# Performance work log

Measured on AMD Instinct MI355X. Metric: run time of the kernel, lower is better.

The kernel has to match this reference:

```python
import jax, jax.numpy as jnp
import numpy as np

N = 50000
E = 800000
DIM = 256
H = 8
D = DIM // H


def setup_inputs() -> dict:
    key = jax.random.key(0)
    ks = jax.random.split(key, 12)
    s = 1.0 / np.sqrt(DIM)
    return {
        "x": jax.random.normal(ks[0], (N, DIM), dtype=jnp.float32),
        "Wq": jax.random.normal(ks[1], (DIM, DIM), dtype=jnp.float32) * s,
        "bq": jax.random.normal(ks[2], (DIM,), dtype=jnp.float32) * 0.01,
        "Wk": jax.random.normal(ks[3], (DIM, DIM), dtype=jnp.float32) * s,
        "bk": jax.random.normal(ks[4], (DIM,), dtype=jnp.float32) * 0.01,
        "Wv": jax.random.normal(ks[5], (DIM, DIM), dtype=jnp.float32) * s,
        "bv": jax.random.normal(ks[6], (DIM,), dtype=jnp.float32) * 0.01,
        "Wo": jax.random.normal(ks[7], (DIM, DIM), dtype=jnp.float32) * s,
        "bo": jax.random.normal(ks[8], (DIM,), dtype=jnp.float32) * 0.01,
        "src": jax.random.randint(ks[9], (E,), 0, N, dtype=jnp.int32),
        "dst": jax.random.randint(ks[10], (E,), 0, N, dtype=jnp.int32),
    }


def reference(x, Wq, bq, Wk, bk, Wv, bv, Wo, bo, src, dst):
    # Linear projections (torch Linear: x @ W.T + b), then [N, H, D]
    q = (x @ Wq.T + bq).reshape(N, H, D)
    k = (x @ Wk.T + bk).reshape(N, H, D)
    v = (x @ Wv.T + bv).reshape(N, H, D)

    # u_dot_v: per-edge dot(queries[src], keys[dst]) -> [E, H]
    scores = jnp.einsum('ehd,ehd->eh', q[src], k[dst]) / jnp.sqrt(jnp.float32(D))

    # edge_softmax over incoming edges of each destination node
    smax = jax.ops.segment_max(scores, dst, num_segments=N)  # [N, H]
    e = jnp.exp(scores - smax[dst])                          # [E, H]
    ssum = jax.ops.segment_sum(e, dst, num_segments=N)       # [N, H]
    probs = e / ssum[dst]                                    # [E, H]

    # u_mul_e_sum: sum over incoming edges of values[src] * probs -> [N, H, D]
    out = jax.ops.segment_sum(v[src] * probs[:, :, None], dst, num_segments=N)

    out = out.reshape(N, DIM)
    return out @ Wo.T + bo  # dropout is identity at p=0 / eval
```

## Files before the change

### kernel.cpp

```cpp
#include <hip/hip_runtime.h>
#include <hip/hip_bf16.h>
#include <math.h>

#define DIMV 256
#define DV 32

typedef __attribute__((ext_vector_type(8))) short bf16x8;
typedef __attribute__((ext_vector_type(4))) float f32x4;

static __device__ __forceinline__ unsigned short f2bf(float f) {
    unsigned x = __float_as_uint(f);
    x += 0x7FFF + ((x >> 16) & 1);
    return (unsigned short)(x >> 16);
}
static __device__ __forceinline__ float bf2f(unsigned short u) {
    return __uint_as_float(((unsigned)u) << 16);
}

static __device__ __forceinline__ void async16(const void* g, void* lds) {
    __builtin_amdgcn_global_load_lds(
        (const __attribute__((address_space(1))) void*)g,
        (__attribute__((address_space(3))) void*)lds, 16, 0, 0);
}


__global__ void cvt_w(const float* __restrict__ Wq, const float* __restrict__ Wk,
                      const float* __restrict__ Wv, const float* __restrict__ Wo,
                      unsigned short* __restrict__ Wcat) {
    const float* W = blockIdx.y == 0 ? Wq : blockIdx.y == 1 ? Wk : blockIdx.y == 2 ? Wv : Wo;
    int i = blockIdx.x * 256 + threadIdx.x;
    float4 v = ((const float4*)W)[i];
    ushort4 o;
    o.x = f2bf(v.x); o.y = f2bf(v.y); o.z = f2bf(v.z); o.w = f2bf(v.w);
    ((ushort4*)(Wcat + (size_t)blockIdx.y * 65536))[i] = o;
}


__global__ void zero_i32(int* __restrict__ p, int n) {
    int i = blockIdx.x * blockDim.x + threadIdx.x;
    if (i < n) p[i] = 0;
}

__global__ void count_deg(const int* __restrict__ dst, int* __restrict__ deg, int E) {
    int i = blockIdx.x * blockDim.x + threadIdx.x;
    if (i < E) atomicAdd(&deg[dst[i]], 1);
}

__global__ void block_sum(const int* __restrict__ deg, int* __restrict__ bsum, int n) {
    __shared__ int sm[256];
    int i = blockIdx.x * 256 + threadIdx.x;
    sm[threadIdx.x] = (i < n) ? deg[i] : 0;
    __syncthreads();
    for (int s = 128; s > 0; s >>= 1) {
        if (threadIdx.x < s) sm[threadIdx.x] += sm[threadIdx.x + s];
        __syncthreads();
    }
    if (threadIdx.x == 0) bsum[blockIdx.x] = sm[0];
}

__global__ void scan_bsum(int* __restrict__ bsum, int nb) {
    if (threadIdx.x == 0) {
        int r = 0;
        for (int i = 0; i < nb; ++i) { int v = bsum[i]; bsum[i] = r; r += v; }
    }
}

__global__ void scan_final(const int* __restrict__ deg, const int* __restrict__ bsum,
                           int* __restrict__ offsets, int* __restrict__ cursor, int n) {
    __shared__ int sm[256];
    int i = blockIdx.x * 256 + threadIdx.x;
    int v = (i < n) ? deg[i] : 0;
    sm[threadIdx.x] = v;
    __syncthreads();
    for (int s = 1; s < 256; s <<= 1) {
        int t = (threadIdx.x >= s) ? sm[threadIdx.x - s] : 0;
        __syncthreads();
        sm[threadIdx.x] += t;
        __syncthreads();
    }
    int excl = sm[threadIdx.x] - v + bsum[blockIdx.x];
    if (i < n) { offsets[i] = excl; cursor[i] = excl; }
    if (i == n - 1) offsets[n] = excl + v;
}

__global__ void scatter_edges(const int* __restrict__ src, const int* __restrict__ dst,
                              int* __restrict__ cursor, int* __restrict__ perm_src, int E) {
    int i = blockIdx.x * blockDim.x + threadIdx.x;
    if (i < E) {
        int pos = atomicAdd(&cursor[dst[i]], 1);
        perm_src[pos] = src[i];
    }
}


template<bool AF32, bool OF32>
__global__ __launch_bounds__(256, 4)
void gemm_fused(const void* __restrict__ Ain,
                const unsigned short* __restrict__ Wcat,
                const float* __restrict__ b0, const float* __restrict__ b1,
                const float* __restrict__ b2,
                void* __restrict__ Cout, int M, int ntiles) {
    __shared__ unsigned short Bls[2][32 * 256];
    const int tid = threadIdx.x;
    const int w = tid >> 6, lane = tid & 63;
    const int rg = w >> 1, cg = w & 1;
    const int lrow = lane & 15, lkg = lane >> 4;
    const int row0 = blockIdx.x * 64;

    {
        const char* gb = (const char*)Wcat;
        #pragma unroll
        for (int i = 0; i < 4; ++i) {
            unsigned o = (unsigned)(i * 4096 + w * 1024 + lane * 16);
            unsigned srcoff = o ^ (((o >> 9) & 7u) << 4);
            async16(gb + srcoff, (char*)&Bls[0][0] + (i * 4096 + w * 1024));
        }
    }

    bf16x8 a[2][8];
    #pragma unroll
    for (int m = 0; m < 2; ++m) {
        int row = row0 + rg * 32 + m * 16 + lrow;
        row = min(row, M - 1);
        if (AF32) {
            const float* ap = (const float*)Ain + (size_t)row * DIMV + lkg * 8;
            #pragma unroll
            for (int k0 = 0; k0 < 8; ++k0) {
                float4 f0 = *(const float4*)(ap + k0 * 32);
                float4 f1 = *(const float4*)(ap + k0 * 32 + 4);
                bf16x8 r;
                r[0] = (short)f2bf(f0.x); r[1] = (short)f2bf(f0.y);
                r[2] = (short)f2bf(f0.z); r[3] = (short)f2bf(f0.w);
                r[4] = (short)f2bf(f1.x); r[5] = (short)f2bf(f1.y);
                r[6] = (short)f2bf(f1.z); r[7] = (short)f2bf(f1.w);
                a[m][k0] = r;
            }
        } else {
            const unsigned short* ap = (const unsigned short*)Ain + (size_t)row * DIMV + lkg * 8;
            #pragma unroll
            for (int k0 = 0; k0 < 8; ++k0)
                a[m][k0] = *(const bf16x8*)(ap + k0 * 32);
        }
    }
    __syncthreads();

    const int c = cg * 16 + lrow;
    for (int t = 0; t < ntiles; ++t) {
        if (t + 1 < ntiles) {
            const char* gb = (const char*)Wcat + (size_t)(t + 1) * 16384;
            #pragma unroll
            for (int i = 0; i < 4; ++i) {
                unsigned o = (unsigned)(i * 4096 + w * 1024 + lane * 16);
                unsigned srcoff = o ^ (((o >> 9) & 7u) << 4);
                async16(gb + srcoff, (char*)&Bls[(t + 1) & 1][0] + (i * 4096 + w * 1024));
            }
        }

        const char* bls = (const char*)&Bls[t & 1][0];
        f32x4 acc0 = {0.f, 0.f, 0.f, 0.f};
        f32x4 acc1 = {0.f, 0.f, 0.f, 0.f};
        #pragma unroll
        for (int k0 = 0; k0 < 8; ++k0) {
            unsigned lin = (unsigned)c * 512 + (unsigned)k0 * 64 + (unsigned)lkg * 16;
            unsigned addr = lin ^ (((unsigned)c & 7u) << 4);
            bf16x8 bf = *(const bf16x8*)(bls + addr);
            acc0 = __builtin_amdgcn_mfma_f32_16x16x32_bf16(a[0][k0], bf, acc0, 0, 0, 0);
            acc1 = __builtin_amdgcn_mfma_f32_16x16x32_bf16(a[1][k0], bf, acc1, 0, 0, 0);
        }

        int mat = t >> 3;
        const float* bp = (mat == 0) ? b0 : (mat == 1 ? b1 : b2);
        int gcol = ((t & 7) << 5) + c;
        float bias = bp[gcol];
        size_t obase = (size_t)mat * M * DIMV;
        #pragma unroll
        for (int m = 0; m < 2; ++m) {
            f32x4 av = m ? acc1 : acc0;
            #pragma unroll
            for (int r = 0; r < 4; ++r) {
                int row = row0 + rg * 32 + m * 16 + lkg * 4 + r;
                if (row < M) {
                    float val = av[r] + bias;
                    if (OF32)
                        ((float*)Cout)[obase + (size_t)row * DIMV + gcol] = val;
                    else
                        ((unsigned short*)Cout)[obase + (size_t)row * DIMV + gcol] = f2bf(val);
                }
            }
        }
        __syncthreads();
    }
}


__global__ __launch_bounds__(256)
void node_attn(const unsigned short* __restrict__ Q, const unsigned short* __restrict__ K,
               const unsigned short* __restrict__ V,
               const int* __restrict__ offsets, const int* __restrict__ perm_src,
               unsigned short* __restrict__ attn, int N) {
    int wid = blockIdx.x * (blockDim.x >> 6) + (threadIdx.x >> 6);
    if (wid >= N) return;
    int lane = threadIdx.x & 63;
    int col = (lane >> 3) * DV + (lane & 7) * 4;
    const float rsD = 0.17677669529663687f;

    ushort4 kr = *(const ushort4*)(K + (size_t)wid * DIMV + col);
    float k0 = bf2f(kr.x) * rsD, k1 = bf2f(kr.y) * rsD;
    float k2 = bf2f(kr.z) * rsD, k3 = bf2f(kr.w) * rsD;

    float mA = -INFINITY, lA = 0.f, aA0 = 0.f, aA1 = 0.f, aA2 = 0.f, aA3 = 0.f;
    float mB = -INFINITY, lB = 0.f, aB0 = 0.f, aB1 = 0.f, aB2 = 0.f, aB3 = 0.f;

    int e0 = offsets[wid], e1 = offsets[wid + 1];
    int p = e0;
    for (; p + 2 <= e1; p += 2) {
        int s0 = perm_src[p];
        int s1 = perm_src[p + 1];
        ushort4 q0 = *(const ushort4*)(Q + (size_t)s0 * DIMV + col);
        ushort4 q1 = *(const ushort4*)(Q + (size_t)s1 * DIMV + col);
        ushort4 v0 = *(const ushort4*)(V + (size_t)s0 * DIMV + col);
        ushort4 v1 = *(const ushort4*)(V + (size_t)s1 * DIMV + col);
        float d0 = bf2f(q0.x) * k0 + bf2f(q0.y) * k1 + bf2f(q0.z) * k2 + bf2f(q0.w) * k3;
        float d1 = bf2f(q1.x) * k0 + bf2f(q1.y) * k1 + bf2f(q1.z) * k2 + bf2f(q1.w) * k3;
        d0 += __shfl_xor(d0, 1); d0 += __shfl_xor(d0, 2); d0 += __shfl_xor(d0, 4);
        d1 += __shfl_xor(d1, 1); d1 += __shfl_xor(d1, 2); d1 += __shfl_xor(d1, 4);

        float mnA = fmaxf(mA, d0);
        float scA = __expf(mA - mnA);
        float peA = __expf(d0 - mnA);
        lA = lA * scA + peA;
        aA0 = aA0 * scA + peA * bf2f(v0.x);
        aA1 = aA1 * scA + peA * bf2f(v0.y);
        aA2 = aA2 * scA + peA * bf2f(v0.z);
        aA3 = aA3 * scA + peA * bf2f(v0.w);
        mA = mnA;

        float mnB = fmaxf(mB, d1);
        float scB = __expf(mB - mnB);
        float peB = __expf(d1 - mnB);
        lB = lB * scB + peB;
        aB0 = aB0 * scB + peB * bf2f(v1.x);
        aB1 = aB1 * scB + peB * bf2f(v1.y);
        aB2 = aB2 * scB + peB * bf2f(v1.z);
        aB3 = aB3 * scB + peB * bf2f(v1.w);
        mB = mnB;
    }
    if (p < e1) {
        int s0 = perm_src[p];
        ushort4 q0 = *(const ushort4*)(Q + (size_t)s0 * DIMV + col);
        ushort4 v0 = *(const ushort4*)(V + (size_t)s0 * DIMV + col);
        float d0 = bf2f(q0.x) * k0 + bf2f(q0.y) * k1 + bf2f(q0.z) * k2 + bf2f(q0.w) * k3;
        d0 += __shfl_xor(d0, 1); d0 += __shfl_xor(d0, 2); d0 += __shfl_xor(d0, 4);
        float mnA = fmaxf(mA, d0);
        float scA = __expf(mA - mnA);
        float peA = __expf(d0 - mnA);
        lA = lA * scA + peA;
        aA0 = aA0 * scA + peA * bf2f(v0.x);
        aA1 = aA1 * scA + peA * bf2f(v0.y);
        aA2 = aA2 * scA + peA * bf2f(v0.z);
        aA3 = aA3 * scA + peA * bf2f(v0.w);
        mA = mnA;
    }

    float mn = fmaxf(mA, mB);
    float scA = (lA > 0.f) ? __expf(mA - mn) : 0.f;
    float scB = (lB > 0.f) ? __expf(mB - mn) : 0.f;
    float l = lA * scA + lB * scB;
    float o0 = aA0 * scA + aB0 * scB;
    float o1 = aA1 * scA + aB1 * scB;
    float o2 = aA2 * scA + aB2 * scB;
    float o3 = aA3 * scA + aB3 * scB;
    float inv = (l > 0.f) ? 1.f / l : 0.f;

    ushort4 o;
    o.x = f2bf(o0 * inv); o.y = f2bf(o1 * inv); o.z = f2bf(o2 * inv); o.w = f2bf(o3 * inv);
    *(ushort4*)(attn + (size_t)wid * DIMV + col) = o;
}


extern "C" void kernel_launch(void* const* d_in, const int* in_sizes, int n_in,
                              void* d_out, int out_size, void* d_ws, size_t ws_size,
                              hipStream_t stream) {
    const float* x  = (const float*)d_in[0];
    const float* Wq = (const float*)d_in[1];
    const float* bq = (const float*)d_in[2];
    const float* Wk = (const float*)d_in[3];
    const float* bk = (const float*)d_in[4];
    const float* Wv = (const float*)d_in[5];
    const float* bv = (const float*)d_in[6];
    const float* Wo = (const float*)d_in[7];
    const float* bo = (const float*)d_in[8];
    const int* src  = (const int*)d_in[9];
    const int* dst  = (const int*)d_in[10];
    int N = in_sizes[0] / DIMV;
    int E = in_sizes[9];
    float* out = (float*)d_out;

    char* p = (char*)d_ws;
    auto alloc = [&](size_t bytes) {
        char* r = p;
        p += (bytes + 255) & ~(size_t)255;
        return r;
    };
    unsigned short* Wcat = (unsigned short*)alloc((size_t)4 * 65536 * 2);
    unsigned short* QKV  = (unsigned short*)alloc((size_t)3 * N * DIMV * 2);
    unsigned short* attn = (unsigned short*)alloc((size_t)N * DIMV * 2);
    int* deg             = (int*)alloc((size_t)N * 4);
    int* offsets         = (int*)alloc((size_t)(N + 1) * 4);
    int* cursor          = (int*)alloc((size_t)N * 4);
    int* perm_src        = (int*)alloc((size_t)E * 4);
    int* bsum            = (int*)alloc((size_t)1024 * 4);

    dim3 gw(64, 4);
    cvt_w<<<gw, 256, 0, stream>>>(Wq, Wk, Wv, Wo, Wcat);

    int nb = (N + 255) / 256;
    zero_i32<<<nb, 256, 0, stream>>>(deg, N);
    count_deg<<<(E + 255) / 256, 256, 0, stream>>>(dst, deg, E);
    block_sum<<<nb, 256, 0, stream>>>(deg, bsum, N);
    scan_bsum<<<1, 64, 0, stream>>>(bsum, nb);
    scan_final<<<nb, 256, 0, stream>>>(deg, bsum, offsets, cursor, N);
    scatter_edges<<<(E + 255) / 256, 256, 0, stream>>>(src, dst, cursor, perm_src, E);

    int gblocks = (N + 63) / 64;
    gemm_fused<true, false><<<gblocks, 256, 0, stream>>>(
        x, Wcat, bq, bk, bv, QKV, N, 24);

    const unsigned short* Qp = QKV;
    const unsigned short* Kp = QKV + (size_t)N * DIMV;
    const unsigned short* Vp = QKV + (size_t)2 * N * DIMV;
    node_attn<<<(N + 3) / 4, 256, 0, stream>>>(Qp, Kp, Vp, offsets, perm_src, attn, N);

    gemm_fused<false, true><<<gblocks, 256, 0, stream>>>(
        attn, Wcat + (size_t)3 * 65536, bo, bo, bo, out, N, 8);
}
```

Measured before the change: 328.3 us.

## Software-pipeline node attention gathers, use exp2, and streamline CSR build

```diff
diff --git a/kernel.cpp b/kernel.cpp
--- a/kernel.cpp
+++ b/kernel.cpp
@@ -7,6 +7,19 @@
 
 typedef __attribute__((ext_vector_type(8))) short bf16x8;
 typedef __attribute__((ext_vector_type(4))) float f32x4;
+
+#if defined(__has_builtin)
+#if __has_builtin(__builtin_amdgcn_exp2f)
+#define EXPS(x) __builtin_amdgcn_exp2f(x)
+#define SCORE_SCALE 0.25503486237f
+#else
+#define EXPS(x) __expf(x)
+#define SCORE_SCALE 0.17677669529663687f
+#endif
+#else
+#define EXPS(x) __expf(x)
+#define SCORE_SCALE 0.17677669529663687f
+#endif
 
 static __device__ __forceinline__ unsigned short f2bf(float f) {
     unsigned x = __float_as_uint(f);
@@ -36,59 +49,52 @@
 }
 
 
-__global__ void zero_i32(int* __restrict__ p, int n) {
-    int i = blockIdx.x * blockDim.x + threadIdx.x;
-    if (i < n) p[i] = 0;
-}
-
 __global__ void count_deg(const int* __restrict__ dst, int* __restrict__ deg, int E) {
-    int i = blockIdx.x * blockDim.x + threadIdx.x;
-    if (i < E) atomicAdd(&deg[dst[i]], 1);
-}
-
-__global__ void block_sum(const int* __restrict__ deg, int* __restrict__ bsum, int n) {
-    __shared__ int sm[256];
-    int i = blockIdx.x * 256 + threadIdx.x;
-    sm[threadIdx.x] = (i < n) ? deg[i] : 0;
+    int i4 = (blockIdx.x * blockDim.x + threadIdx.x) << 2;
+    if (i4 + 4 <= E) {
+        int4 d = *(const int4*)(dst + i4);
+        atomicAdd(&deg[d.x], 1); atomicAdd(&deg[d.y], 1);
+        atomicAdd(&deg[d.z], 1); atomicAdd(&deg[d.w], 1);
+    } else {
+        for (int j = i4; j < E; ++j) atomicAdd(&deg[dst[j]], 1);
+    }
+}
+
+__global__ __launch_bounds__(1024)
+void scan_offsets(const int* __restrict__ deg, int* __restrict__ offsets,
+                  int* __restrict__ cursor, int n) {
+    __shared__ int sm[1024];
+    int t = threadIdx.x;
+    int chunk = (n + 1023) >> 10;
+    int lo = min(t * chunk, n), hi = min(lo + chunk, n);
+    int s = 0;
+    for (int i = lo; i < hi; ++i) s += deg[i];
+    sm[t] = s;
     __syncthreads();
-    for (int s = 128; s > 0; s >>= 1) {
-        if (threadIdx.x < s) sm[threadIdx.x] += sm[threadIdx.x + s];
+    for (int st = 1; st < 1024; st <<= 1) {
+        int v = (t >= st) ? sm[t - st] : 0;
         __syncthreads();
-    }
-    if (threadIdx.x == 0) bsum[blockIdx.x] = sm[0];
-}
-
-__global__ void scan_bsum(int* __restrict__ bsum, int nb) {
-    if (threadIdx.x == 0) {
-        int r = 0;
-        for (int i = 0; i < nb; ++i) { int v = bsum[i]; bsum[i] = r; r += v; }
-    }
-}
-
-__global__ void scan_final(const int* __restrict__ deg, const int* __restrict__ bsum,
-                           int* __restrict__ offsets, int* __restrict__ cursor, int n) {
-    __shared__ int sm[256];
-    int i = blockIdx.x * 256 + threadIdx.x;
-    int v = (i < n) ? deg[i] : 0;
-    sm[threadIdx.x] = v;
-    __syncthreads();
-    for (int s = 1; s < 256; s <<= 1) {
-        int t = (threadIdx.x >= s) ? sm[threadIdx.x - s] : 0;
+        sm[t] += v;
         __syncthreads();
-        sm[threadIdx.x] += t;
-        __syncthreads();
-    }
-    int excl = sm[threadIdx.x] - v + bsum[blockIdx.x];
-    if (i < n) { offsets[i] = excl; cursor[i] = excl; }
-    if (i == n - 1) offsets[n] = excl + v;
+    }
+    int run = sm[t] - s;
+    for (int i = lo; i < hi; ++i) { offsets[i] = run; cursor[i] = run; run += deg[i]; }
+    if (t == 1023) offsets[n] = run;
 }
 
 __global__ void scatter_edges(const int* __restrict__ src, const int* __restrict__ dst,
                               int* __restrict__ cursor, int* __restrict__ perm_src, int E) {
-    int i = blockIdx.x * blockDim.x + threadIdx.x;
-    if (i < E) {
-        int pos = atomicAdd(&cursor[dst[i]], 1);
-        perm_src[pos] = src[i];
+    int i4 = (blockIdx.x * blockDim.x + threadIdx.x) << 2;
+    if (i4 + 4 <= E) {
+        int4 d = *(const int4*)(dst + i4);
+        int4 s = *(const int4*)(src + i4);
+        perm_src[atomicAdd(&cursor[d.x], 1)] = s.x;
+        perm_src[atomicAdd(&cursor[d.y], 1)] = s.y;
+        perm_src[atomicAdd(&cursor[d.z], 1)] = s.z;
+        perm_src[atomicAdd(&cursor[d.w], 1)] = s.w;
+    } else {
+        for (int j = i4; j < E; ++j)
+            perm_src[atomicAdd(&cursor[dst[j]], 1)] = src[j];
     }
 }
 
@@ -202,69 +208,80 @@
     if (wid >= N) return;
     int lane = threadIdx.x & 63;
     int col = (lane >> 3) * DV + (lane & 7) * 4;
-    const float rsD = 0.17677669529663687f;
 
     ushort4 kr = *(const ushort4*)(K + (size_t)wid * DIMV + col);
-    float k0 = bf2f(kr.x) * rsD, k1 = bf2f(kr.y) * rsD;
-    float k2 = bf2f(kr.z) * rsD, k3 = bf2f(kr.w) * rsD;
+    float k0 = bf2f(kr.x) * SCORE_SCALE, k1 = bf2f(kr.y) * SCORE_SCALE;
+    float k2 = bf2f(kr.z) * SCORE_SCALE, k3 = bf2f(kr.w) * SCORE_SCALE;
 
     float mA = -INFINITY, lA = 0.f, aA0 = 0.f, aA1 = 0.f, aA2 = 0.f, aA3 = 0.f;
     float mB = -INFINITY, lB = 0.f, aB0 = 0.f, aB1 = 0.f, aB2 = 0.f, aB3 = 0.f;
 
+    auto upd = [&](ushort4 qr, ushort4 vr, float& m, float& l,
+                   float& a0, float& a1, float& a2, float& a3) {
+        float d = bf2f(qr.x) * k0 + bf2f(qr.y) * k1 + bf2f(qr.z) * k2 + bf2f(qr.w) * k3;
+        d += __shfl_xor(d, 1); d += __shfl_xor(d, 2); d += __shfl_xor(d, 4);
+        float mn = fmaxf(m, d);
+        float sc = EXPS(m - mn);
+        float pe = EXPS(d - mn);
+        l = l * sc + pe;
+        a0 = a0 * sc + pe * bf2f(vr.x);
+        a1 = a1 * sc + pe * bf2f(vr.y);
+        a2 = a2 * sc + pe * bf2f(vr.z);
+        a3 = a3 * sc + pe * bf2f(vr.w);
+        m = mn;
+    };
+
     int e0 = offsets[wid], e1 = offsets[wid + 1];
+    int rem = e1 - e0;
+    int S = rem >> 1;
     int p = e0;
-    for (; p + 2 <= e1; p += 2) {
-        int s0 = perm_src[p];
-        int s1 = perm_src[p + 1];
-        ushort4 q0 = *(const ushort4*)(Q + (size_t)s0 * DIMV + col);
-        ushort4 q1 = *(const ushort4*)(Q + (size_t)s1 * DIMV + col);
-        ushort4 v0 = *(const ushort4*)(V + (size_t)s0 * DIMV + col);
-        ushort4 v1 = *(const ushort4*)(V + (size_t)s1 * DIMV + col);
-        float d0 = bf2f(q0.x) * k0 + bf2f(q0.y) * k1 + bf2f(q0.z) * k2 + bf2f(q0.w) * k3;
-        float d1 = bf2f(q1.x) * k0 + bf2f(q1.y) * k1 + bf2f(q1.z) * k2 + bf2f(q1.w) * k3;
-        d0 += __shfl_xor(d0, 1); d0 += __shfl_xor(d0, 2); d0 += __shfl_xor(d0, 4);
-        d1 += __shfl_xor(d1, 1); d1 += __shfl_xor(d1, 2); d1 += __shfl_xor(d1, 4);
-
-        float mnA = fmaxf(mA, d0);
-        float scA = __expf(mA - mnA);
-        float peA = __expf(d0 - mnA);
-        lA = lA * scA + peA;
-        aA0 = aA0 * scA + peA * bf2f(v0.x);
-        aA1 = aA1 * scA + peA * bf2f(v0.y);
-        aA2 = aA2 * scA + peA * bf2f(v0.z);
-        aA3 = aA3 * scA + peA * bf2f(v0.w);
-        mA = mnA;
-
-        float mnB = fmaxf(mB, d1);
-        float scB = __expf(mB - mnB);
-        float peB = __expf(d1 - mnB);
-        lB = lB * scB + peB;
-        aB0 = aB0 * scB + peB * bf2f(v1.x);
-        aB1 = aB1 * scB + peB * bf2f(v1.y);
-        aB2 = aB2 * scB + peB * bf2f(v1.z);
-        aB3 = aB3 * scB + peB * bf2f(v1.w);
-        mB = mnB;
-    }
-    if (p < e1) {
-        int s0 = perm_src[p];
-        ushort4 q0 = *(const ushort4*)(Q + (size_t)s0 * DIMV + col);
-        ushort4 v0 = *(const ushort4*)(V + (size_t)s0 * DIMV + col);
-        float d0 = bf2f(q0.x) * k0 + bf2f(q0.y) * k1 + bf2f(q0.z) * k2 + bf2f(q0.w) * k3;
-        d0 += __shfl_xor(d0, 1); d0 += __shfl_xor(d0, 2); d0 += __shfl_xor(d0, 4);
-        float mnA = fmaxf(mA, d0);
-        float scA = __expf(mA - mnA);
-        float peA = __expf(d0 - mnA);
-        lA = lA * scA + peA;
-        aA0 = aA0 * scA + peA * bf2f(v0.x);
-        aA1 = aA1 * scA + peA * bf2f(v0.y);
-        aA2 = aA2 * scA + peA * bf2f(v0.z);
-        aA3 = aA3 * scA + peA * bf2f(v0.w);
-        mA = mnA;
+
+    if (S >= 1) {
+        int i0 = perm_src[p], i1 = perm_src[p + 1];
+        ushort4 qA0 = *(const ushort4*)(Q + (size_t)i0 * DIMV + col);
+        ushort4 qA1 = *(const ushort4*)(Q + (size_t)i1 * DIMV + col);
+        ushort4 vA0 = *(const ushort4*)(V + (size_t)i0 * DIMV + col);
+        ushort4 vA1 = *(const ushort4*)(V + (size_t)i1 * DIMV + col);
+        int n0 = 0, n1 = 0;
+        if (S >= 2) { n0 = perm_src[p + 2]; n1 = perm_src[p + 3]; }
+        ushort4 qB0, qB1, vB0, vB1;
+
+        int s = 0;
+        while (s + 2 <= S) {
+            qB0 = *(const ushort4*)(Q + (size_t)n0 * DIMV + col);
+            qB1 = *(const ushort4*)(Q + (size_t)n1 * DIMV + col);
+            vB0 = *(const ushort4*)(V + (size_t)n0 * DIMV + col);
+            vB1 = *(const ushort4*)(V + (size_t)n1 * DIMV + col);
+            if (s + 2 < S) { n0 = perm_src[p + 2 * s + 4]; n1 = perm_src[p + 2 * s + 5]; }
+            upd(qA0, vA0, mA, lA, aA0, aA1, aA2, aA3);
+            upd(qA1, vA1, mB, lB, aB0, aB1, aB2, aB3);
+
+            if (s + 2 < S) {
+                qA0 = *(const ushort4*)(Q + (size_t)n0 * DIMV + col);
+                qA1 = *(const ushort4*)(Q + (size_t)n1 * DIMV + col);
+                vA0 = *(const ushort4*)(V + (size_t)n0 * DIMV + col);
+                vA1 = *(const ushort4*)(V + (size_t)n1 * DIMV + col);
+                if (s + 3 < S) { n0 = perm_src[p + 2 * s + 6]; n1 = perm_src[p + 2 * s + 7]; }
+            }
+            upd(qB0, vB0, mA, lA, aA0, aA1, aA2, aA3);
+            upd(qB1, vB1, mB, lB, aB0, aB1, aB2, aB3);
+            s += 2;
+        }
+        if (s < S) {
+            upd(qA0, vA0, mA, lA, aA0, aA1, aA2, aA3);
+            upd(qA1, vA1, mB, lB, aB0, aB1, aB2, aB3);
+        }
+    }
+    if (rem & 1) {
+        int i0 = perm_src[e1 - 1];
+        ushort4 q0 = *(const ushort4*)(Q + (size_t)i0 * DIMV + col);
+        ushort4 v0 = *(const ushort4*)(V + (size_t)i0 * DIMV + col);
+        upd(q0, v0, mA, lA, aA0, aA1, aA2, aA3);
     }
 
     float mn = fmaxf(mA, mB);
-    float scA = (lA > 0.f) ? __expf(mA - mn) : 0.f;
-    float scB = (lB > 0.f) ? __expf(mB - mn) : 0.f;
+    float scA = (lA > 0.f) ? EXPS(mA - mn) : 0.f;
+    float scB = (lB > 0.f) ? EXPS(mB - mn) : 0.f;
     float l = lA * scA + lB * scB;
     float o0 = aA0 * scA + aB0 * scB;
     float o1 = aA1 * scA + aB1 * scB;
@@ -309,18 +326,15 @@
     int* offsets         = (int*)alloc((size_t)(N + 1) * 4);
     int* cursor          = (int*)alloc((size_t)N * 4);
     int* perm_src        = (int*)alloc((size_t)E * 4);
-    int* bsum            = (int*)alloc((size_t)1024 * 4);
 
     dim3 gw(64, 4);
     cvt_w<<<gw, 256, 0, stream>>>(Wq, Wk, Wv, Wo, Wcat);
 
-    int nb = (N + 255) / 256;
-    zero_i32<<<nb, 256, 0, stream>>>(deg, N);
-    count_deg<<<(E + 255) / 256, 256, 0, stream>>>(dst, deg, E);
-    block_sum<<<nb, 256, 0, stream>>>(deg, bsum, N);
-    scan_bsum<<<1, 64, 0, stream>>>(bsum, nb);
-    scan_final<<<nb, 256, 0, stream>>>(deg, bsum, offsets, cursor, N);
-    scatter_edges<<<(E + 255) / 256, 256, 0, stream>>>(src, dst, cursor, perm_src, E);
+    hipMemsetAsync(deg, 0, (size_t)N * 4, stream);
+    int e4blocks = ((E + 3) / 4 + 255) / 256;
+    count_deg<<<e4blocks, 256, 0, stream>>>(dst, deg, E);
+    scan_offsets<<<1, 1024, 0, stream>>>(deg, offsets, cursor, N);
+    scatter_edges<<<e4blocks, 256, 0, stream>>>(src, dst, cursor, perm_src, E);
 
     int gblocks = (N + 63) / 64;
     gemm_fused<true, false><<<gblocks, 256, 0, stream>>>(
```

After: 407.8 us. 1.24x slower.

## Interleave Q/K/V per node and software-pipeline gathers in node attention

Applied to the files above, without the earlier changes.

```diff
diff --git a/kernel.cpp b/kernel.cpp
--- a/kernel.cpp
+++ b/kernel.cpp
@@ -4,9 +4,13 @@
 
 #define DIMV 256
 #define DV 32
+#define QKVS 768
 
 typedef __attribute__((ext_vector_type(8))) short bf16x8;
 typedef __attribute__((ext_vector_type(4))) float f32x4;
+
+#define EXPS(x) __expf(x)
+#define SCORE_SCALE 0.17677669529663687f
 
 static __device__ __forceinline__ unsigned short f2bf(float f) {
     unsigned x = __float_as_uint(f);
@@ -93,7 +97,7 @@
 }
 
 
-template<bool AF32, bool OF32>
+template<bool AF32, bool OF32, int OSTRIDE, int MATSTRIDE>
 __global__ __launch_bounds__(256, 4)
 void gemm_fused(const void* __restrict__ Ain,
                 const unsigned short* __restrict__ Wcat,
@@ -172,7 +176,7 @@
         const float* bp = (mat == 0) ? b0 : (mat == 1 ? b1 : b2);
         int gcol = ((t & 7) << 5) + c;
         float bias = bp[gcol];
-        size_t obase = (size_t)mat * M * DIMV;
+        unsigned cbase = (unsigned)mat * MATSTRIDE + gcol;
         #pragma unroll
         for (int m = 0; m < 2; ++m) {
             f32x4 av = m ? acc1 : acc0;
@@ -182,9 +186,9 @@
                 if (row < M) {
                     float val = av[r] + bias;
                     if (OF32)
-                        ((float*)Cout)[obase + (size_t)row * DIMV + gcol] = val;
+                        ((float*)Cout)[(size_t)row * OSTRIDE + cbase] = val;
                     else
-                        ((unsigned short*)Cout)[obase + (size_t)row * DIMV + gcol] = f2bf(val);
+                        ((unsigned short*)Cout)[(size_t)row * OSTRIDE + cbase] = f2bf(val);
                 }
             }
         }
@@ -194,77 +198,97 @@
 
 
 __global__ __launch_bounds__(256)
-void node_attn(const unsigned short* __restrict__ Q, const unsigned short* __restrict__ K,
-               const unsigned short* __restrict__ V,
+void node_attn(const unsigned short* __restrict__ QKV,
                const int* __restrict__ offsets, const int* __restrict__ perm_src,
                unsigned short* __restrict__ attn, int N) {
     int wid = blockIdx.x * (blockDim.x >> 6) + (threadIdx.x >> 6);
     if (wid >= N) return;
     int lane = threadIdx.x & 63;
-    int col = (lane >> 3) * DV + (lane & 7) * 4;
-    const float rsD = 0.17677669529663687f;
-
-    ushort4 kr = *(const ushort4*)(K + (size_t)wid * DIMV + col);
-    float k0 = bf2f(kr.x) * rsD, k1 = bf2f(kr.y) * rsD;
-    float k2 = bf2f(kr.z) * rsD, k3 = bf2f(kr.w) * rsD;
+    unsigned col = (unsigned)((lane >> 3) * DV + (lane & 7) * 4);
+
+    ushort4 kr = *(const ushort4*)(QKV + (size_t)wid * QKVS + 256 + col);
+    float k0 = bf2f(kr.x) * SCORE_SCALE, k1 = bf2f(kr.y) * SCORE_SCALE;
+    float k2 = bf2f(kr.z) * SCORE_SCALE, k3 = bf2f(kr.w) * SCORE_SCALE;
 
     float mA = -INFINITY, lA = 0.f, aA0 = 0.f, aA1 = 0.f, aA2 = 0.f, aA3 = 0.f;
     float mB = -INFINITY, lB = 0.f, aB0 = 0.f, aB1 = 0.f, aB2 = 0.f, aB3 = 0.f;
 
+    auto upd = [&](ushort4 qr, ushort4 vr, float& m, float& l,
+                   float& a0, float& a1, float& a2, float& a3) {
+        float d = bf2f(qr.x) * k0 + bf2f(qr.y) * k1 + bf2f(qr.z) * k2 + bf2f(qr.w) * k3;
+        d += __shfl_xor(d, 1); d += __shfl_xor(d, 2); d += __shfl_xor(d, 4);
+        float mn = fmaxf(m, d);
+        float sc = EXPS(m - mn);
+        float pe = EXPS(d - mn);
+        l = l * sc + pe;
+        a0 = a0 * sc + pe * bf2f(vr.x);
+        a1 = a1 * sc + pe * bf2f(vr.y);
+        a2 = a2 * sc + pe * bf2f(vr.z);
+        a3 = a3 * sc + pe * bf2f(vr.w);
+        m = mn;
+    };
+
     int e0 = offsets[wid], e1 = offsets[wid + 1];
+    int rem = e1 - e0;
+    int S = rem >> 1;
     int p = e0;
-    for (; p + 2 <= e1; p += 2) {
-        int s0 = perm_src[p];
-        int s1 = perm_src[p + 1];
-        ushort4 q0 = *(const ushort4*)(Q + (size_t)s0 * DIMV + col);
-        ushort4 q1 = *(const ushort4*)(Q + (size_t)s1 * DIMV + col);
-        ushort4 v0 = *(const ushort4*)(V + (size_t)s0 * DIMV + col);
-        ushort4 v1 = *(const ushort4*)(V + (size_t)s1 * DIMV + col);
-        float d0 = bf2f(q0.x) * k0 + bf2f(q0.y) * k1 + bf2f(q0.z) * k2 + bf2f(q0.w) * k3;
-        float d1 = bf2f(q1.x) * k0 + bf2f(q1.y) * k1 + bf2f(q1.z) * k2 + bf2f(q1.w) * k3;
-        d0 += __shfl_xor(d0, 1); d0 += __shfl_xor(d0, 2); d0 += __shfl_xor(d0, 4);
-        d1 += __shfl_xor(d1, 1); d1 += __shfl_xor(d1, 2); d1 += __shfl_xor(d1, 4);
-
-        float mnA = fmaxf(mA, d0);
-        float scA = __expf(mA - mnA);
-        float peA = __expf(d0 - mnA);
-        lA = lA * scA + peA;
-        aA0 = aA0 * scA + peA * bf2f(v0.x);
-        aA1 = aA1 * scA + peA * bf2f(v0.y);
-        aA2 = aA2 * scA + peA * bf2f(v0.z);
-        aA3 = aA3 * scA + peA * bf2f(v0.w);
-        mA = mnA;
-
-        float mnB = fmaxf(mB, d1);
-        float scB = __expf(mB - mnB);
-        float peB = __expf(d1 - mnB);
-        lB = lB * scB + peB;
-        aB0 = aB0 * scB + peB * bf2f(v1.x);
-        aB1 = aB1 * scB + peB * bf2f(v1.y);
-        aB2 = aB2 * scB + peB * bf2f(v1.z);
-        aB3 = aB3 * scB + peB * bf2f(v1.w);
-        mB = mnB;
-    }
-    if (p < e1) {
-        int s0 = perm_src[p];
-        ushort4 q0 = *(const ushort4*)(Q + (size_t)s0 * DIMV + col);
-        ushort4 v0 = *(const ushort4*)(V + (size_t)s0 * DIMV + col);
-        float d0 = bf2f(q0.x) * k0 + bf2f(q0.y) * k1 + bf2f(q0.z) * k2 + bf2f(q0.w) * k3;
-        d0 += __shfl_xor(d0, 1); d0 += __shfl_xor(d0, 2); d0 += __shfl_xor(d0, 4);
-        float mnA = fmaxf(mA, d0);
-        float scA = __expf(mA - mnA);
-        float peA = __expf(d0 - mnA);
-        lA = lA * scA + peA;
-        aA0 = aA0 * scA + peA * bf2f(v0.x);
-        aA1 = aA1 * scA + peA * bf2f(v0.y);
-        aA2 = aA2 * scA + peA * bf2f(v0.z);
-        aA3 = aA3 * scA + peA * bf2f(v0.w);
-        mA = mnA;
+
+    if (S >= 1) {
+        unsigned o0 = (unsigned)perm_src[p] * QKVS + col;
+        unsigned o1 = (unsigned)perm_src[p + 1] * QKVS + col;
+        ushort4 qA0 = *(const ushort4*)(QKV + o0);
+        ushort4 vA0 = *(const ushort4*)(QKV + o0 + 512);
+        ushort4 qA1 = *(const ushort4*)(QKV + o1);
+        ushort4 vA1 = *(const ushort4*)(QKV + o1 + 512);
+        unsigned n0 = 0, n1 = 0;
+        if (S >= 2) {
+            n0 = (unsigned)perm_src[p + 2] * QKVS + col;
+            n1 = (unsigned)perm_src[p + 3] * QKVS + col;
+        }
+        ushort4 qB0, qB1, vB0, vB1;
+
+        int s = 0;
+        while (s + 2 <= S) {
+            qB0 = *(const ushort4*)(QKV + n0);
+            vB0 = *(const ushort4*)(QKV + n0 + 512);
+            qB1 = *(const ushort4*)(QKV + n1);
+            vB1 = *(const ushort4*)(QKV + n1 + 512);
+            if (s + 2 < S) {
+                n0 = (unsigned)perm_src[p + 2 * s + 4] * QKVS + col;
+                n1 = (unsigned)perm_src[p + 2 * s + 5] * QKVS + col;
+            }
+            upd(qA0, vA0, mA, lA, aA0, aA1, aA2, aA3);
+            upd(qA1, vA1, mB, lB, aB0, aB1, aB2, aB3);
+
+            if (s + 2 < S) {
+                qA0 = *(const ushort4*)(QKV + n0);
+                vA0 = *(const ushort4*)(QKV + n0 + 512);
+                qA1 = *(const ushort4*)(QKV + n1);
+                vA1 = *(const ushort4*)(QKV + n1 + 512);
+                if (s + 3 < S) {
+                    n0 = (unsigned)perm_src[p + 2 * s + 6] * QKVS + col;
+                    n1 = (unsigned)perm_src[p + 2 * s + 7] * QKVS + col;
+                }
+            }
+            upd(qB0, vB0, mA, lA, aA0, aA1, aA2, aA3);
+            upd(qB1, vB1, mB, lB, aB0, aB1, aB2, aB3);
+            s += 2;
+        }
+        if (s < S) {
+            upd(qA0, vA0, mA, lA, aA0, aA1, aA2, aA3);
+            upd(qA1, vA1, mB, lB, aB0, aB1, aB2, aB3);
+        }
+    }
+    if (rem & 1) {
+        unsigned o0 = (unsigned)perm_src[e1 - 1] * QKVS + col;
+        ushort4 q0 = *(const ushort4*)(QKV + o0);
+        ushort4 v0 = *(const ushort4*)(QKV + o0 + 512);
+        upd(q0, v0, mA, lA, aA0, aA1, aA2, aA3);
     }
 
     float mn = fmaxf(mA, mB);
-    float scA = (lA > 0.f) ? __expf(mA - mn) : 0.f;
-    float scB = (lB > 0.f) ? __expf(mB - mn) : 0.f;
+    float scA = (lA > 0.f) ? EXPS(mA - mn) : 0.f;
+    float scB = (lB > 0.f) ? EXPS(mB - mn) : 0.f;
     float l = lA * scA + lB * scB;
     float o0 = aA0 * scA + aB0 * scB;
     float o1 = aA1 * scA + aB1 * scB;
@@ -303,7 +327,7 @@
         return r;
     };
     unsigned short* Wcat = (unsigned short*)alloc((size_t)4 * 65536 * 2);
-    unsigned short* QKV  = (unsigned short*)alloc((size_t)3 * N * DIMV * 2);
+    unsigned short* QKV  = (unsigned short*)alloc((size_t)N * QKVS * 2);
     unsigned short* attn = (unsigned short*)alloc((size_t)N * DIMV * 2);
     int* deg             = (int*)alloc((size_t)N * 4);
     int* offsets         = (int*)alloc((size_t)(N + 1) * 4);
@@ -323,14 +347,11 @@
     scatter_edges<<<(E + 255) / 256, 256, 0, stream>>>(src, dst, cursor, perm_src, E);
 
     int gblocks = (N + 63) / 64;
-    gemm_fused<true, false><<<gblocks, 256, 0, stream>>>(
+    gemm_fused<true, false, QKVS, 256><<<gblocks, 256, 0, stream>>>(
         x, Wcat, bq, bk, bv, QKV, N, 24);
 
-    const unsigned short* Qp = QKV;
-    const unsigned short* Kp = QKV + (size_t)N * DIMV;
-    const unsigned short* Vp = QKV + (size_t)2 * N * DIMV;
-    node_attn<<<(N + 3) / 4, 256, 0, stream>>>(Qp, Kp, Vp, offsets, perm_src, attn, N);
-
-    gemm_fused<false, true><<<gblocks, 256, 0, stream>>>(
+    node_attn<<<(N + 3) / 4, 256, 0, stream>>>(QKV, offsets, perm_src, attn, N);
+
+    gemm_fused<false, true, DIMV, 0><<<gblocks, 256, 0, stream>>>(
         attn, Wcat + (size_t)3 * 65536, bo, bo, bo, out, N, 8);
 }
```

After: 326.7 us. No clear change (-0.5%).
